# Kernel optimization log

Hardware: AMD Instinct MI355X
Metric: run time of the kernel (lower is better)

The kernel has to match this reference:

```python
import jax, jax.numpy as jnp
import numpy as np

DIM = 1024
INTER = 512
E = 16            # n_routed_experts
TOPK = 4          # n_activated_experts
N_GROUPS = 4
TOPK_GROUPS = 2
ROUTE_SCALE = 1.0
INIT_STD = 0.02
B, S = 2, 1024


def setup_inputs() -> dict:
    key = jax.random.key(0)
    ks = jax.random.split(key, 8)
    return {
        "x": jax.random.normal(ks[0], (B, S, DIM), jnp.float32),
        "gate_w": jax.random.normal(ks[1], (E, DIM), jnp.float32) * INIT_STD,
        "gate_bias": jnp.zeros((E,), jnp.float32),
        "w1": jax.random.normal(ks[2], (E, INTER, DIM), jnp.float32) * INIT_STD,
        "w2": jax.random.normal(ks[3], (E, DIM, INTER), jnp.float32) * INIT_STD,
        "w3": jax.random.normal(ks[4], (E, INTER, DIM), jnp.float32) * INIT_STD,
        "ws1": jax.random.normal(ks[5], (INTER, DIM), jnp.float32) * INIT_STD,
        "ws2": jax.random.normal(ks[6], (DIM, INTER), jnp.float32) * INIT_STD,
        "ws3": jax.random.normal(ks[7], (INTER, DIM), jnp.float32) * INIT_STD,
    }


def reference(x, gate_w, gate_bias, w1, w2, w3, ws1, ws2, ws3):
    Bx, Sx, D = x.shape
    T = Bx * Sx
    xf = x.reshape(T, D)

    # ---- Gate: sigmoid scores + expert bias, group-limited top-k ----
    scores = jax.nn.sigmoid(xf @ gate_w.T)          # [T, E]
    original_scores = scores
    s = scores + gate_bias                          # bias only affects selection
    sg = s.reshape(T, N_GROUPS, E // N_GROUPS)
    group_scores = sg.max(axis=-1)                  # [T, G]
    _, gidx = jax.lax.top_k(group_scores, TOPK_GROUPS)
    keep = jnp.zeros((T, N_GROUPS), bool).at[jnp.arange(T)[:, None], gidx].set(True)
    s_masked = jnp.where(keep[:, :, None], sg, -jnp.inf).reshape(T, E)
    _, idx = jax.lax.top_k(s_masked, TOPK)          # [T, topk]
    weights = jnp.take_along_axis(original_scores, idx, axis=1) * ROUTE_SCALE

    # combine weights as sparse [T, E] matrix (scatter of top-k weights)
    comb = jnp.zeros((T, E), x.dtype).at[jnp.arange(T)[:, None], idx].add(weights)

    # ---- Routed experts: SwiGLU per expert, weighted combine ----
    h1 = jnp.einsum('td,eid->tei', xf, w1)          # [T, E, inter]
    h3 = jnp.einsum('td,eid->tei', xf, w3)
    h = jax.nn.silu(h1) * h3
    y = jnp.einsum('tei,edi,te->td', h, w2, comb)   # weighted combine

    # ---- Shared expert (SwiGLU MLP) ----
    z = (jax.nn.silu(xf @ ws1.T) * (xf @ ws3.T)) @ ws2.T

    return (y + z).reshape(Bx, Sx, D)
```

## Files before the change

### kernel.cpp

```cpp
#include <hip/hip_runtime.h>

#define T_TOK  2048
#define DIMD   1024
#define INTERI 512
#define NEXP   16
#define NSEG   17

typedef __bf16 bf16x8 __attribute__((ext_vector_type(8)));
typedef float  f32x4  __attribute__((ext_vector_type(4)));
typedef float  f32x8  __attribute__((ext_vector_type(8)));
typedef unsigned short u16x8 __attribute__((ext_vector_type(8)));

#define SW(row, c) ((((c) + ((row) >> 1)) & 3) * 8)

__device__ __forceinline__ unsigned short f2b(float f) {
    union { float f; unsigned int u; } c; c.f = f;
    unsigned int u = c.u;
    unsigned int r = (u + 0x7FFFu + ((u >> 16) & 1u)) >> 16;
    return (unsigned short)r;
}

__device__ __forceinline__ bf16x8 cvt8(f32x8 v) {
    bf16x8 r;
#pragma unroll
    for (int i = 0; i < 8; ++i) r[i] = (__bf16)v[i];
    return r;
}

__device__ __forceinline__ void lds_barrier() {
    asm volatile("s_waitcnt lgkmcnt(0)" ::: "memory");
    __builtin_amdgcn_s_barrier();
}

__global__ __launch_bounds__(256) void cvt_w_kernel(
    const float* __restrict__ w1,  const float* __restrict__ w3,
    const float* __restrict__ ws1, const float* __restrict__ ws3,
    unsigned short* __restrict__ w1b,  unsigned short* __restrict__ w3b,
    unsigned short* __restrict__ ws1b, unsigned short* __restrict__ ws3b)
{
    int g = blockIdx.x * 256 + threadIdx.x;
    const float* s; unsigned short* d; int i;
    if      (g < 1048576) { s = w1;  d = w1b;  i = g; }
    else if (g < 2097152) { s = w3;  d = w3b;  i = g - 1048576; }
    else if (g < 2162688) { s = ws1; d = ws1b; i = g - 2097152; }
    else                  { s = ws3; d = ws3b; i = g - 2162688; }
    float4 v0 = ((const float4*)s)[2 * i];
    float4 v1 = ((const float4*)s)[2 * i + 1];
    u16x8 o;
    o[0] = f2b(v0.x); o[1] = f2b(v0.y); o[2] = f2b(v0.z); o[3] = f2b(v0.w);
    o[4] = f2b(v1.x); o[5] = f2b(v1.y); o[6] = f2b(v1.z); o[7] = f2b(v1.w);
    ((u16x8*)d)[i] = o;
}

__global__ __launch_bounds__(256) void gate_score_kernel(
    const float* __restrict__ x, const float* __restrict__ gw,
    const float* __restrict__ gb,
    unsigned* __restrict__ sel, float4* __restrict__ selw,
    unsigned short* __restrict__ xb)
{
    int tok  = blockIdx.x * 4 + (threadIdx.x >> 6);
    int lane = threadIdx.x & 63;
    const float* xp = x + (size_t)tok * DIMD;
    float xv[16];
#pragma unroll
    for (int j = 0; j < 16; ++j) xv[j] = xp[j * 64 + lane];

    unsigned short* xbp = xb + (size_t)tok * DIMD;
#pragma unroll
    for (int j = 0; j < 16; ++j) xbp[j * 64 + lane] = f2b(xv[j]);

    float sc[16];
#pragma unroll
    for (int e = 0; e < 16; ++e) {
        const float* gwe = gw + e * DIMD;
        float p0 = 0.f, p1 = 0.f;
#pragma unroll
        for (int j = 0; j < 16; j += 2) {
            p0 += xv[j]     * gwe[j * 64 + lane];
            p1 += xv[j + 1] * gwe[(j + 1) * 64 + lane];
        }
        float p = p0 + p1;
#pragma unroll
        for (int o = 32; o; o >>= 1) p += __shfl_xor(p, o, 64);
        sc[e] = p;
    }
    if (lane != 0) return;

    float orig[16], s[16];
#pragma unroll
    for (int e = 0; e < 16; ++e) {
        orig[e] = 1.f / (1.f + expf(-sc[e]));
        s[e] = orig[e] + gb[e];
    }
    float gmax[4];
#pragma unroll
    for (int g = 0; g < 4; ++g) {
        float m = s[4 * g];
        for (int j = 1; j < 4; ++j) m = fmaxf(m, s[4 * g + j]);
        gmax[g] = m;
    }
    int g0 = 0;
    for (int g = 1; g < 4; ++g) if (gmax[g] > gmax[g0]) g0 = g;
    int g1 = -1;
    for (int g = 0; g < 4; ++g) { if (g == g0) continue; if (g1 < 0 || gmax[g] > gmax[g1]) g1 = g; }
    unsigned keep = (0xFu << (4 * g0)) | (0xFu << (4 * g1));
    unsigned used = 0;
    unsigned pk = 0;
    float w4[4];
    for (int j = 0; j < 4; ++j) {
        int best = -1;
        for (int e = 0; e < 16; ++e) {
            if (!((keep >> e) & 1u) || ((used >> e) & 1u)) continue;
            if (best < 0 || s[e] > s[best]) best = e;
        }
        used |= 1u << best;
        pk |= ((unsigned)best) << (4 * j);
        w4[j] = orig[best];
    }
    sel[tok] = pk;
    selw[tok] = make_float4(w4[0], w4[1], w4[2], w4[3]);
}

__global__ __launch_bounds__(256) void build_lists_kernel(
    const unsigned* __restrict__ sel, const float4* __restrict__ selw,
    int* __restrict__ counts, int* __restrict__ lst, float* __restrict__ lstw)
{
    const int e    = blockIdx.x;
    const int tid  = threadIdx.x;
    const int wave = tid >> 6;
    const int lane = tid & 63;

    __shared__ int wsum[4];
    __shared__ int basev;
    if (tid == 0) basev = 0;
    __syncthreads();

    for (int c = 0; c < T_TOK / 256; ++c) {
        int t = c * 256 + tid;
        unsigned s = sel[t];
        int match = -1;
#pragma unroll
        for (int j = 0; j < 4; ++j)
            if (((s >> (4 * j)) & 15u) == (unsigned)e) match = j;
        unsigned long long m = __ballot(match >= 0);
        int wpre = __popcll(m & ((1ull << lane) - 1ull));
        if (lane == 0) wsum[wave] = __popcll(m);
        __syncthreads();
        int pre = basev;
        for (int wv = 0; wv < wave; ++wv) pre += wsum[wv];
        if (match >= 0) {
            int pos = pre + wpre;
            lst [e * T_TOK + pos] = t | (match << 16);
            const float* wp = (const float*)&selw[t];
            lstw[e * T_TOK + pos] = wp[match];
        }
        __syncthreads();
        if (tid == 0) basev += wsum[0] + wsum[1] + wsum[2] + wsum[3];
        __syncthreads();
    }
    if (tid == 0) counts[e] = basev;
}

__global__ __launch_bounds__(256, 2) void gemm1_kernel(
    const unsigned short* __restrict__ xb,
    const unsigned short* __restrict__ w1b,
    const unsigned short* __restrict__ w3b,
    const unsigned short* __restrict__ ws1b,
    const unsigned short* __restrict__ ws3b,
    const int* __restrict__ counts,
    const int* __restrict__ lst,
    unsigned short* __restrict__ H)
{
    int b = blockIdx.x;
    int seg, mt, nt;
    if (b < 1024) {
        int xcd = b & 7, slot = b >> 3;
        seg = xcd + 8 * (slot >> 6);
        int tile = slot & 63;
        mt = tile >> 2; nt = tile & 3;
    } else {
        seg = NEXP;
        int tile = b - 1024;
        mt = tile >> 2; nt = tile & 3;
    }
    const int n_e = (seg == NEXP) ? T_TOK : counts[seg];
    const int m0  = mt * 128;
    if (m0 >= n_e) return;
    const int n0  = nt * 128;

    const unsigned short* w1p = (seg == NEXP) ? ws1b : w1b + (size_t)seg * INTERI * DIMD;
    const unsigned short* w3p = (seg == NEXP) ? ws3b : w3b + (size_t)seg * INTERI * DIMD;
    const int* lste = lst + seg * T_TOK;

    __shared__ __align__(16) unsigned short lA [2][128][32];
    __shared__ __align__(16) unsigned short lB1[2][128][32];
    __shared__ __align__(16) unsigned short lB3[2][128][32];

    const int tid  = threadIdx.x;
    const int wave = tid >> 6;
    const int lane = tid & 63;
    const int quad = lane >> 4;
    const int lrow = lane & 15;
    const int r4   = tid >> 2;
    const int ct   = tid & 3;

    int ra0 = m0 + r4;       if (ra0 > n_e - 1) ra0 = n_e - 1;
    int ra1 = m0 + r4 + 64;  if (ra1 > n_e - 1) ra1 = n_e - 1;
    int tok0 = (seg == NEXP) ? ra0 : (lste[ra0] & 0xFFFF);
    int tok1 = (seg == NEXP) ? ra1 : (lste[ra1] & 0xFFFF);
    const unsigned short* gA0  = xb  + (size_t)tok0 * DIMD + ct * 8;
    const unsigned short* gA1  = xb  + (size_t)tok1 * DIMD + ct * 8;
    const unsigned short* gB1a = w1p + (size_t)(n0 + r4)      * DIMD + ct * 8;
    const unsigned short* gB1b = w1p + (size_t)(n0 + r4 + 64) * DIMD + ct * 8;
    const unsigned short* gB3a = w3p + (size_t)(n0 + r4)      * DIMD + ct * 8;
    const unsigned short* gB3b = w3p + (size_t)(n0 + r4 + 64) * DIMD + ct * 8;

    bf16x8 pa[2][2], pb1[2][2], pb3[2][2];

#define G1LOAD(k0) do { _Pragma("unroll") for (int kk = 0; kk < 2; ++kk) { \
    pa [0][kk] = *(const bf16x8*)(gA0  + (k0) + kk * 32); \
    pa [1][kk] = *(const bf16x8*)(gA1  + (k0) + kk * 32); \
    pb1[0][kk] = *(const bf16x8*)(gB1a + (k0) + kk * 32); \
    pb1[1][kk] = *(const bf16x8*)(gB1b + (k0) + kk * 32); \
    pb3[0][kk] = *(const bf16x8*)(gB3a + (k0) + kk * 32); \
    pb3[1][kk] = *(const bf16x8*)(gB3b + (k0) + kk * 32); } } while (0)

#define G1STORE() do { _Pragma("unroll") for (int kk = 0; kk < 2; ++kk) { \
    *(bf16x8*)&lA [kk][r4]     [SW(r4, ct)]      = pa [0][kk]; \
    *(bf16x8*)&lA [kk][64 + r4][SW(64 + r4, ct)] = pa [1][kk]; \
    *(bf16x8*)&lB1[kk][r4]     [SW(r4, ct)]      = pb1[0][kk]; \
    *(bf16x8*)&lB1[kk][64 + r4][SW(64 + r4, ct)] = pb1[1][kk]; \
    *(bf16x8*)&lB3[kk][r4]     [SW(r4, ct)]      = pb3[0][kk]; \
    *(bf16x8*)&lB3[kk][64 + r4][SW(64 + r4, ct)] = pb3[1][kk]; } } while (0)

    f32x4 acc1[4][4], acc3[4][4];
    const f32x4 zero = {0.f, 0.f, 0.f, 0.f};
#pragma unroll
    for (int i = 0; i < 4; ++i)
#pragma unroll
        for (int j = 0; j < 4; ++j) { acc1[i][j] = zero; acc3[i][j] = zero; }

    const int wm = (wave & 1) * 64;
    const int wn = (wave >> 1) * 64;

    G1LOAD(0);
    const int NK = DIMD / 64;
    for (int it = 0; it < NK; ++it) {
        G1STORE();
        lds_barrier();
        if (it + 1 < NK) G1LOAD((it + 1) * 64);
#pragma unroll
        for (int kk = 0; kk < 2; ++kk) {
            bf16x8 a[4], b1[4], b3[4];
#pragma unroll
            for (int t = 0; t < 4; ++t) {
                int rr = wm + t * 16 + lrow;
                a[t] = *(const bf16x8*)&lA[kk][rr][SW(rr, quad)];
            }
#pragma unroll
            for (int t = 0; t < 4; ++t) {
                int rc = wn + t * 16 + lrow;
                b1[t] = *(const bf16x8*)&lB1[kk][rc][SW(rc, quad)];
                b3[t] = *(const bf16x8*)&lB3[kk][rc][SW(rc, quad)];
            }
#pragma unroll
            for (int i = 0; i < 4; ++i)
#pragma unroll
                for (int j = 0; j < 4; ++j) {
                    acc1[i][j] = __builtin_amdgcn_mfma_f32_16x16x32_bf16(a[i], b1[j], acc1[i][j], 0, 0, 0);
                    acc3[i][j] = __builtin_amdgcn_mfma_f32_16x16x32_bf16(a[i], b3[j], acc3[i][j], 0, 0, 0);
                }
        }
        lds_barrier();
    }
#undef G1LOAD
#undef G1STORE

    unsigned short* Hseg = H + (size_t)seg * T_TOK * INTERI;
#pragma unroll
    for (int i = 0; i < 4; ++i) {
        int rbase = m0 + wm + i * 16 + quad * 4;
#pragma unroll
        for (int r = 0; r < 4; ++r) {
            int row = rbase + r;
            if (row >= n_e) continue;
            unsigned short* hrow = Hseg + (size_t)row * INTERI + n0 + wn + lrow;
#pragma unroll
            for (int j = 0; j < 4; ++j) {
                float v1 = acc1[i][j][r];
                float v3 = acc3[i][j][r];
                float hv = (v1 / (1.f + __expf(-v1))) * v3;
                hrow[j * 16] = f2b(hv);
            }
        }
    }
}

__global__ __launch_bounds__(256, 2) void gemm2_kernel(
    const unsigned short* __restrict__ H,
    const float* __restrict__ w2f,
    const float* __restrict__ ws2f,
    const int* __restrict__ counts,
    const int* __restrict__ lst,
    const float* __restrict__ lstw,
    float* __restrict__ P)
{
    int b = blockIdx.x;
    int seg, mt, nt;
    if (b < 2048) {
        int xcd = b & 7, slot = b >> 3;
        seg = xcd + 8 * (slot >> 7);
        int tile = slot & 127;
        mt = tile >> 3; nt = tile & 7;
    } else {
        seg = NEXP;
        int tile = b - 2048;
        mt = tile >> 3; nt = tile & 7;
    }
    const int n_e = (seg == NEXP) ? T_TOK : counts[seg];
    const int m0  = mt * 128;
    if (m0 >= n_e) return;
    const int n0  = nt * 128;

    const float* w2p = (seg == NEXP) ? ws2f : w2f + (size_t)seg * DIMD * INTERI;
    const unsigned short* Hseg = H + (size_t)seg * T_TOK * INTERI;

    __shared__ __align__(16) unsigned short lA[2][128][32];
    __shared__ __align__(16) unsigned short lB[2][128][32];

    const int tid  = threadIdx.x;
    const int wave = tid >> 6;
    const int lane = tid & 63;
    const int quad = lane >> 4;
    const int lrow = lane & 15;
    const int r4   = tid >> 2;
    const int ct   = tid & 3;

    int ra0 = m0 + r4;       if (ra0 > n_e - 1) ra0 = n_e - 1;
    int ra1 = m0 + r4 + 64;  if (ra1 > n_e - 1) ra1 = n_e - 1;
    const unsigned short* gA0 = Hseg + (size_t)ra0 * INTERI + ct * 8;
    const unsigned short* gA1 = Hseg + (size_t)ra1 * INTERI + ct * 8;
    const float* gB0 = w2p + (size_t)(n0 + r4)      * INTERI + ct * 8;
    const float* gB1 = w2p + (size_t)(n0 + r4 + 64) * INTERI + ct * 8;

    bf16x8 pa[2][2];
    f32x8  pb[2][2];

#define G2LOAD(k0) do { _Pragma("unroll") for (int kk = 0; kk < 2; ++kk) { \
    pa[0][kk] = *(const bf16x8*)(gA0 + (k0) + kk * 32); \
    pa[1][kk] = *(const bf16x8*)(gA1 + (k0) + kk * 32); \
    pb[0][kk] = *(const f32x8*)(gB0 + (k0) + kk * 32); \
    pb[1][kk] = *(const f32x8*)(gB1 + (k0) + kk * 32); } } while (0)

#define G2STORE() do { _Pragma("unroll") for (int kk = 0; kk < 2; ++kk) { \
    *(bf16x8*)&lA[kk][r4]     [SW(r4, ct)]      = pa[0][kk]; \
    *(bf16x8*)&lA[kk][64 + r4][SW(64 + r4, ct)] = pa[1][kk]; \
    *(bf16x8*)&lB[kk][r4]     [SW(r4, ct)]      = cvt8(pb[0][kk]); \
    *(bf16x8*)&lB[kk][64 + r4][SW(64 + r4, ct)] = cvt8(pb[1][kk]); } } while (0)

    f32x4 acc[4][4];
    const f32x4 zero = {0.f, 0.f, 0.f, 0.f};
#pragma unroll
    for (int i = 0; i < 4; ++i)
#pragma unroll
        for (int j = 0; j < 4; ++j) acc[i][j] = zero;

    const int wm = (wave & 1) * 64;
    const int wn = (wave >> 1) * 64;

    G2LOAD(0);
    const int NK = INTERI / 64;
    for (int it = 0; it < NK; ++it) {
        G2STORE();
        lds_barrier();
        if (it + 1 < NK) G2LOAD((it + 1) * 64);
#pragma unroll
        for (int kk = 0; kk < 2; ++kk) {
            bf16x8 a[4], bv[4];
#pragma unroll
            for (int t = 0; t < 4; ++t) {
                int rr = wm + t * 16 + lrow;
                a[t] = *(const bf16x8*)&lA[kk][rr][SW(rr, quad)];
            }
#pragma unroll
            for (int t = 0; t < 4; ++t) {
                int rc = wn + t * 16 + lrow;
                bv[t] = *(const bf16x8*)&lB[kk][rc][SW(rc, quad)];
            }
#pragma unroll
            for (int i = 0; i < 4; ++i)
#pragma unroll
                for (int j = 0; j < 4; ++j)
                    acc[i][j] = __builtin_amdgcn_mfma_f32_16x16x32_bf16(a[i], bv[j], acc[i][j], 0, 0, 0);
        }
        lds_barrier();
    }
#undef G2LOAD
#undef G2STORE

#pragma unroll
    for (int i = 0; i < 4; ++i) {
        int rbase = m0 + wm + i * 16 + quad * 4;
#pragma unroll
        for (int r = 0; r < 4; ++r) {
            int row = rbase + r;
            if (row >= n_e) continue;
            int tok, slot; float wt;
            if (seg == NEXP) { tok = row; slot = 4; wt = 1.f; }
            else {
                int ent = lst[seg * T_TOK + row];
                tok = ent & 0xFFFF; slot = ent >> 16;
                wt = lstw[seg * T_TOK + row];
            }
            float* prow = P + ((size_t)slot * T_TOK + tok) * DIMD + n0 + wn + lrow;
#pragma unroll
            for (int j = 0; j < 4; ++j)
                prow[j * 16] = wt * acc[i][j][r];
        }
    }
}

__global__ __launch_bounds__(256) void combine_kernel(
    const float4* __restrict__ P, float4* __restrict__ y)
{
    const int i = blockIdx.x * 256 + threadIdx.x;
    const size_t plane = (size_t)T_TOK * DIMD / 4;
    float4 a = P[i];
    float4 b = P[plane + i];
    float4 c = P[2 * plane + i];
    float4 d = P[3 * plane + i];
    float4 e = P[4 * plane + i];
    float4 o;
    o.x = a.x + b.x + c.x + d.x + e.x;
    o.y = a.y + b.y + c.y + d.y + e.y;
    o.z = a.z + b.z + c.z + d.z + e.z;
    o.w = a.w + b.w + c.w + d.w + e.w;
    y[i] = o;
}

extern "C" void kernel_launch(void* const* d_in, const int* in_sizes, int n_in,
                              void* d_out, int out_size, void* d_ws, size_t ws_size,
                              hipStream_t stream)
{
    const float* x   = (const float*)d_in[0];
    const float* gw  = (const float*)d_in[1];
    const float* gb  = (const float*)d_in[2];
    const float* w1  = (const float*)d_in[3];
    const float* w2  = (const float*)d_in[4];
    const float* w3  = (const float*)d_in[5];
    const float* ws1 = (const float*)d_in[6];
    const float* ws2 = (const float*)d_in[7];
    const float* ws3 = (const float*)d_in[8];

    char* base = (char*)d_ws;
    size_t off = 0;
    auto alloc = [&](size_t bytes) {
        char* q = base + off; off += (bytes + 255) & ~(size_t)255; return q;
    };
    unsigned short* xb   = (unsigned short*)alloc((size_t)T_TOK * DIMD * 2);
    unsigned short* w1b  = (unsigned short*)alloc((size_t)NEXP * INTERI * DIMD * 2);
    unsigned short* w3b  = (unsigned short*)alloc((size_t)NEXP * INTERI * DIMD * 2);
    unsigned short* ws1b = (unsigned short*)alloc((size_t)INTERI * DIMD * 2);
    unsigned short* ws3b = (unsigned short*)alloc((size_t)INTERI * DIMD * 2);
    unsigned short* Hb   = (unsigned short*)alloc((size_t)NSEG * T_TOK * INTERI * 2);
    int*            cnts = (int*)alloc(NEXP * 4);
    int*            lstp = (int*)alloc((size_t)NEXP * T_TOK * 4);
    float*          lstw = (float*)alloc((size_t)NEXP * T_TOK * 4);
    unsigned*       selp = (unsigned*)alloc((size_t)T_TOK * 4);
    float4*         selw = (float4*)alloc((size_t)T_TOK * 16);
    float*          Pb   = (float*)alloc((size_t)5 * T_TOK * DIMD * 4);

    cvt_w_kernel<<<8704, 256, 0, stream>>>(w1, w3, ws1, ws3, w1b, w3b, ws1b, ws3b);
    gate_score_kernel<<<T_TOK / 4, 256, 0, stream>>>(x, gw, gb, selp, selw, xb);
    build_lists_kernel<<<NEXP, 256, 0, stream>>>(selp, selw, cnts, lstp, lstw);
    gemm1_kernel<<<1088, 256, 0, stream>>>(xb, w1b, w3b, ws1b, ws3b, cnts, lstp, Hb);
    gemm2_kernel<<<2176, 256, 0, stream>>>(Hb, w2, ws2, cnts, lstp, lstw, Pb);
    combine_kernel<<<(T_TOK * DIMD / 4) / 256, 256, 0, stream>>>((const float4*)Pb, (float4*)d_out);
}
```

Measured before the change: 247.5 us.

## Fuse prep kernels, compute expert lists per block, atomically accumulate output

Merges weight conversion, gating and output zeroing into one prep launch. The separate list-building kernel is dropped: each GEMM block rescans the selection array to build its own 128-row token window in shared memory. The 5-plane partial buffer and its combine kernel are replaced by float atomic adds into the output. This removes launches and about 40 MB of partial-buffer traffic, but adds a serial 2048-token scan with barriers in every GEMM block and atomic contention on the output.

```diff
diff --git a/kernel.cpp b/kernel.cpp
--- a/kernel.cpp
+++ b/kernel.cpp
@@ -32,33 +32,40 @@
     __builtin_amdgcn_s_barrier();
 }
 
-__global__ __launch_bounds__(256) void cvt_w_kernel(
+__global__ __launch_bounds__(256) void prep_kernel(
     const float* __restrict__ w1,  const float* __restrict__ w3,
     const float* __restrict__ ws1, const float* __restrict__ ws3,
     unsigned short* __restrict__ w1b,  unsigned short* __restrict__ w3b,
-    unsigned short* __restrict__ ws1b, unsigned short* __restrict__ ws3b)
-{
-    int g = blockIdx.x * 256 + threadIdx.x;
-    const float* s; unsigned short* d; int i;
-    if      (g < 1048576) { s = w1;  d = w1b;  i = g; }
-    else if (g < 2097152) { s = w3;  d = w3b;  i = g - 1048576; }
-    else if (g < 2162688) { s = ws1; d = ws1b; i = g - 2097152; }
-    else                  { s = ws3; d = ws3b; i = g - 2162688; }
-    float4 v0 = ((const float4*)s)[2 * i];
-    float4 v1 = ((const float4*)s)[2 * i + 1];
-    u16x8 o;
-    o[0] = f2b(v0.x); o[1] = f2b(v0.y); o[2] = f2b(v0.z); o[3] = f2b(v0.w);
-    o[4] = f2b(v1.x); o[5] = f2b(v1.y); o[6] = f2b(v1.z); o[7] = f2b(v1.w);
-    ((u16x8*)d)[i] = o;
-}
-
-__global__ __launch_bounds__(256) void gate_score_kernel(
+    unsigned short* __restrict__ ws1b, unsigned short* __restrict__ ws3b,
     const float* __restrict__ x, const float* __restrict__ gw,
     const float* __restrict__ gb,
     unsigned* __restrict__ sel, float4* __restrict__ selw,
-    unsigned short* __restrict__ xb)
+    unsigned short* __restrict__ xb,
+    float4* __restrict__ yzero)
 {
-    int tok  = blockIdx.x * 4 + (threadIdx.x >> 6);
+    const int b = blockIdx.x;
+    if (b < 8704) {
+        int g = b * 256 + threadIdx.x;
+        const float* s; unsigned short* d; int i;
+        if      (g < 1048576) { s = w1;  d = w1b;  i = g; }
+        else if (g < 2097152) { s = w3;  d = w3b;  i = g - 1048576; }
+        else if (g < 2162688) { s = ws1; d = ws1b; i = g - 2097152; }
+        else                  { s = ws3; d = ws3b; i = g - 2162688; }
+        float4 v0 = ((const float4*)s)[2 * i];
+        float4 v1 = ((const float4*)s)[2 * i + 1];
+        u16x8 o;
+        o[0] = f2b(v0.x); o[1] = f2b(v0.y); o[2] = f2b(v0.z); o[3] = f2b(v0.w);
+        o[4] = f2b(v1.x); o[5] = f2b(v1.y); o[6] = f2b(v1.z); o[7] = f2b(v1.w);
+        ((u16x8*)d)[i] = o;
+        return;
+    }
+    if (b >= 9216) {
+        size_t i = (size_t)(b - 9216) * 256 + threadIdx.x;
+        float4 z; z.x = 0.f; z.y = 0.f; z.z = 0.f; z.w = 0.f;
+        yzero[i] = z;
+        return;
+    }
+    int tok  = (b - 8704) * 4 + (threadIdx.x >> 6);
     int lane = threadIdx.x & 63;
     const float* xp = x + (size_t)tok * DIMD;
     float xv[16];
@@ -121,44 +128,45 @@
     selw[tok] = make_float4(w4[0], w4[1], w4[2], w4[3]);
 }
 
-__global__ __launch_bounds__(256) void build_lists_kernel(
+__device__ __forceinline__ int scan_expert_window(
     const unsigned* __restrict__ sel, const float4* __restrict__ selw,
-    int* __restrict__ counts, int* __restrict__ lst, float* __restrict__ lstw)
+    int seg, int m0, int* l_tok, float* l_wt,
+    int* wsum, int* l_cnt)
 {
-    const int e    = blockIdx.x;
     const int tid  = threadIdx.x;
     const int wave = tid >> 6;
     const int lane = tid & 63;
-
-    __shared__ int wsum[4];
-    __shared__ int basev;
-    if (tid == 0) basev = 0;
+    if (tid == 0) *l_cnt = 0;
     __syncthreads();
-
     for (int c = 0; c < T_TOK / 256; ++c) {
         int t = c * 256 + tid;
         unsigned s = sel[t];
         int match = -1;
 #pragma unroll
         for (int j = 0; j < 4; ++j)
-            if (((s >> (4 * j)) & 15u) == (unsigned)e) match = j;
+            if (((s >> (4 * j)) & 15u) == (unsigned)seg) match = j;
         unsigned long long m = __ballot(match >= 0);
         int wpre = __popcll(m & ((1ull << lane) - 1ull));
         if (lane == 0) wsum[wave] = __popcll(m);
         __syncthreads();
-        int pre = basev;
+        int pre = *l_cnt;
         for (int wv = 0; wv < wave; ++wv) pre += wsum[wv];
         if (match >= 0) {
             int pos = pre + wpre;
-            lst [e * T_TOK + pos] = t | (match << 16);
-            const float* wp = (const float*)&selw[t];
-            lstw[e * T_TOK + pos] = wp[match];
+            int rel = pos - m0;
+            if (rel >= 0 && rel < 128) {
+                l_tok[rel] = t | (match << 16);
+                if (l_wt) {
+                    const float* wp = (const float*)&selw[t];
+                    l_wt[rel] = wp[match];
+                }
+            }
         }
         __syncthreads();
-        if (tid == 0) basev += wsum[0] + wsum[1] + wsum[2] + wsum[3];
+        if (tid == 0) *l_cnt += wsum[0] + wsum[1] + wsum[2] + wsum[3];
         __syncthreads();
     }
-    if (tid == 0) counts[e] = basev;
+    return *l_cnt;
 }
 
 __global__ __launch_bounds__(256, 2) void gemm1_kernel(
@@ -167,8 +175,7 @@
     const unsigned short* __restrict__ w3b,
     const unsigned short* __restrict__ ws1b,
     const unsigned short* __restrict__ ws3b,
-    const int* __restrict__ counts,
-    const int* __restrict__ lst,
+    const unsigned* __restrict__ sel,
     unsigned short* __restrict__ H)
 {
     int b = blockIdx.x;
@@ -183,18 +190,23 @@
         int tile = b - 1024;
         mt = tile >> 2; nt = tile & 3;
     }
-    const int n_e = (seg == NEXP) ? T_TOK : counts[seg];
     const int m0  = mt * 128;
-    if (m0 >= n_e) return;
     const int n0  = nt * 128;
-
-    const unsigned short* w1p = (seg == NEXP) ? ws1b : w1b + (size_t)seg * INTERI * DIMD;
-    const unsigned short* w3p = (seg == NEXP) ? ws3b : w3b + (size_t)seg * INTERI * DIMD;
-    const int* lste = lst + seg * T_TOK;
 
     __shared__ __align__(16) unsigned short lA [2][128][32];
     __shared__ __align__(16) unsigned short lB1[2][128][32];
     __shared__ __align__(16) unsigned short lB3[2][128][32];
+    __shared__ int l_tok[128];
+    __shared__ int wsum[4];
+    __shared__ int l_cnt;
+
+    int n_e;
+    if (seg == NEXP) n_e = T_TOK;
+    else n_e = scan_expert_window(sel, nullptr, seg, m0, l_tok, nullptr, wsum, &l_cnt);
+    if (m0 >= n_e) return;
+
+    const unsigned short* w1p = (seg == NEXP) ? ws1b : w1b + (size_t)seg * INTERI * DIMD;
+    const unsigned short* w3p = (seg == NEXP) ? ws3b : w3b + (size_t)seg * INTERI * DIMD;
 
     const int tid  = threadIdx.x;
     const int wave = tid >> 6;
@@ -206,8 +218,8 @@
 
     int ra0 = m0 + r4;       if (ra0 > n_e - 1) ra0 = n_e - 1;
     int ra1 = m0 + r4 + 64;  if (ra1 > n_e - 1) ra1 = n_e - 1;
-    int tok0 = (seg == NEXP) ? ra0 : (lste[ra0] & 0xFFFF);
-    int tok1 = (seg == NEXP) ? ra1 : (lste[ra1] & 0xFFFF);
+    int tok0 = (seg == NEXP) ? ra0 : (l_tok[ra0 - m0] & 0xFFFF);
+    int tok1 = (seg == NEXP) ? ra1 : (l_tok[ra1 - m0] & 0xFFFF);
     const unsigned short* gA0  = xb  + (size_t)tok0 * DIMD + ct * 8;
     const unsigned short* gA1  = xb  + (size_t)tok1 * DIMD + ct * 8;
     const unsigned short* gB1a = w1p + (size_t)(n0 + r4)      * DIMD + ct * 8;
@@ -300,10 +312,9 @@
     const unsigned short* __restrict__ H,
     const float* __restrict__ w2f,
     const float* __restrict__ ws2f,
-    const int* __restrict__ counts,
-    const int* __restrict__ lst,
-    const float* __restrict__ lstw,
-    float* __restrict__ P)
+    const unsigned* __restrict__ sel,
+    const float4* __restrict__ selw,
+    float* __restrict__ y)
 {
     int b = blockIdx.x;
     int seg, mt, nt;
@@ -317,16 +328,23 @@
         int tile = b - 2048;
         mt = tile >> 3; nt = tile & 7;
     }
-    const int n_e = (seg == NEXP) ? T_TOK : counts[seg];
     const int m0  = mt * 128;
+    const int n0  = nt * 128;
+
+    __shared__ __align__(16) unsigned short lA[2][128][32];
+    __shared__ __align__(16) unsigned short lB[2][128][32];
+    __shared__ int   l_tok[128];
+    __shared__ float l_wt[128];
+    __shared__ int   wsum[4];
+    __shared__ int   l_cnt;
+
+    int n_e;
+    if (seg == NEXP) n_e = T_TOK;
+    else n_e = scan_expert_window(sel, selw, seg, m0, l_tok, l_wt, wsum, &l_cnt);
     if (m0 >= n_e) return;
-    const int n0  = nt * 128;
 
     const float* w2p = (seg == NEXP) ? ws2f : w2f + (size_t)seg * DIMD * INTERI;
     const unsigned short* Hseg = H + (size_t)seg * T_TOK * INTERI;
-
-    __shared__ __align__(16) unsigned short lA[2][128][32];
-    __shared__ __align__(16) unsigned short lB[2][128][32];
 
     const int tid  = threadIdx.x;
     const int wave = tid >> 6;
@@ -405,37 +423,19 @@
         for (int r = 0; r < 4; ++r) {
             int row = rbase + r;
             if (row >= n_e) continue;
-            int tok, slot; float wt;
-            if (seg == NEXP) { tok = row; slot = 4; wt = 1.f; }
+            int tok; float wt;
+            if (seg == NEXP) { tok = row; wt = 1.f; }
             else {
-                int ent = lst[seg * T_TOK + row];
-                tok = ent & 0xFFFF; slot = ent >> 16;
-                wt = lstw[seg * T_TOK + row];
-            }
-            float* prow = P + ((size_t)slot * T_TOK + tok) * DIMD + n0 + wn + lrow;
+                int ent = l_tok[row - m0];
+                tok = ent & 0xFFFF;
+                wt  = l_wt[row - m0];
+            }
+            float* yrow = y + (size_t)tok * DIMD + n0 + wn + lrow;
 #pragma unroll
             for (int j = 0; j < 4; ++j)
-                prow[j * 16] = wt * acc[i][j][r];
-        }
-    }
-}
-
-__global__ __launch_bounds__(256) void combine_kernel(
-    const float4* __restrict__ P, float4* __restrict__ y)
-{
-    const int i = blockIdx.x * 256 + threadIdx.x;
-    const size_t plane = (size_t)T_TOK * DIMD / 4;
-    float4 a = P[i];
-    float4 b = P[plane + i];
-    float4 c = P[2 * plane + i];
-    float4 d = P[3 * plane + i];
-    float4 e = P[4 * plane + i];
-    float4 o;
-    o.x = a.x + b.x + c.x + d.x + e.x;
-    o.y = a.y + b.y + c.y + d.y + e.y;
-    o.z = a.z + b.z + c.z + d.z + e.z;
-    o.w = a.w + b.w + c.w + d.w + e.w;
-    y[i] = o;
+                unsafeAtomicAdd(&yrow[j * 16], wt * acc[i][j][r]);
+        }
+    }
 }
 
 extern "C" void kernel_launch(void* const* d_in, const int* in_sizes, int n_in,
@@ -463,17 +463,13 @@
     unsigned short* ws1b = (unsigned short*)alloc((size_t)INTERI * DIMD * 2);
     unsigned short* ws3b = (unsigned short*)alloc((size_t)INTERI * DIMD * 2);
     unsigned short* Hb   = (unsigned short*)alloc((size_t)NSEG * T_TOK * INTERI * 2);
-    int*            cnts = (int*)alloc(NEXP * 4);
-    int*            lstp = (int*)alloc((size_t)NEXP * T_TOK * 4);
-    float*          lstw = (float*)alloc((size_t)NEXP * T_TOK * 4);
     unsigned*       selp = (unsigned*)alloc((size_t)T_TOK * 4);
     float4*         selw = (float4*)alloc((size_t)T_TOK * 16);
-    float*          Pb   = (float*)alloc((size_t)5 * T_TOK * DIMD * 4);
-
-    cvt_w_kernel<<<8704, 256, 0, stream>>>(w1, w3, ws1, ws3, w1b, w3b, ws1b, ws3b);
-    gate_score_kernel<<<T_TOK / 4, 256, 0, stream>>>(x, gw, gb, selp, selw, xb);
-    build_lists_kernel<<<NEXP, 256, 0, stream>>>(selp, selw, cnts, lstp, lstw);
-    gemm1_kernel<<<1088, 256, 0, stream>>>(xb, w1b, w3b, ws1b, ws3b, cnts, lstp, Hb);
-    gemm2_kernel<<<2176, 256, 0, stream>>>(Hb, w2, ws2, cnts, lstp, lstw, Pb);
-    combine_kernel<<<(T_TOK * DIMD / 4) / 256, 256, 0, stream>>>((const float4*)Pb, (float4*)d_out);
-}
+
+    prep_kernel<<<11264, 256, 0, stream>>>(w1, w3, ws1, ws3,
+                                           w1b, w3b, ws1b, ws3b,
+                                           x, gw, gb, selp, selw, xb,
+                                           (float4*)d_out);
+    gemm1_kernel<<<1088, 256, 0, stream>>>(xb, w1b, w3b, ws1b, ws3b, selp, Hb);
+    gemm2_kernel<<<2176, 256, 0, stream>>>(Hb, w2, ws2, selp, selw, (float*)d_out);
+}
```

Result: slower. 279.8 us (+13.1%).
